# Optimization experiments

Measured on AMD Instinct MI355X. Metric: run time of the kernel, lower is better.

The kernel has to match this reference:

```python
import jax, jax.numpy as jnp
import numpy as np

NT, NP = 100000, 20000
FT, FP, H = 128, 64, 128
E, EL = 2000000, 500000
EPS = 1e-12


def _l2norm(x):
    # F.normalize(x, p=2, dim=-1): x / max(||x||, eps)
    n = jnp.sqrt(jnp.sum(x * x, axis=-1, keepdims=True))
    return x / jnp.maximum(n, EPS)


def _seg_mean(x_src, src_idx, dst_idx, n_dst, inv_cnt):
    # gather src features per edge, scatter-sum to dst, divide by in-degree
    s = jax.ops.segment_sum(x_src[src_idx], dst_idx, num_segments=n_dst)
    return s * inv_cnt[:, None]


def setup_inputs() -> dict:
    key = jax.random.key(0)
    ks = jax.random.split(key, 24)

    def w(k, fan_in, fan_out):
        return jax.random.normal(k, (fan_in, fan_out), jnp.float32) / np.sqrt(fan_in)

    inp = {
        "x_track": jax.random.normal(ks[0], (NT, FT), jnp.float32),
        "x_playlist": jax.random.normal(ks[1], (NP, FP), jnp.float32),
        "edge_src": jax.random.randint(ks[2], (E,), 0, NT),
        "edge_dst": jax.random.randint(ks[3], (E,), 0, NP),
        "label_src": jax.random.randint(ks[4], (EL,), 0, NT),
        "label_dst": jax.random.randint(ks[5], (EL,), 0, NP),
        # per-type input projections (PyG Linear, bias=True)
        "Wn_t": w(ks[6], FT, H), "bn_t": jnp.zeros((H,), jnp.float32),
        "Wn_p": w(ks[7], FP, H), "bn_p": jnp.zeros((H,), jnp.float32),
        # layer1: edge type track->playlist (dst playlist) and reverse (dst track)
        "W1_l_p": w(ks[8], H, H), "b1_p": jnp.zeros((H,), jnp.float32), "W1_r_p": w(ks[9], H, H),
        "W1_l_t": w(ks[10], H, H), "b1_t": jnp.zeros((H,), jnp.float32), "W1_r_t": w(ks[11], H, H),
        # layer2
        "W2_l_p": w(ks[12], H, H), "b2_p": jnp.zeros((H,), jnp.float32), "W2_r_p": w(ks[13], H, H),
        "W2_l_t": w(ks[14], H, H), "b2_t": jnp.zeros((H,), jnp.float32), "W2_r_t": w(ks[15], H, H),
    }
    return inp


def reference(x_track, x_playlist, edge_src, edge_dst, label_src, label_dst,
              Wn_t, bn_t, Wn_p, bn_p,
              W1_l_p, b1_p, W1_r_p, W1_l_t, b1_t, W1_r_t,
              W2_l_p, b2_p, W2_r_p, W2_l_t, b2_t, W2_r_t):
    nt, np_ = x_track.shape[0], x_playlist.shape[0]
    ones = jnp.ones(edge_src.shape, jnp.float32)
    inv_cnt_p = 1.0 / jnp.maximum(jax.ops.segment_sum(ones, edge_dst, num_segments=np_), 1.0)
    inv_cnt_t = 1.0 / jnp.maximum(jax.ops.segment_sum(ones, edge_src, num_segments=nt), 1.0)

    # per-type input linear
    h_t = x_track @ Wn_t + bn_t        # [NT, H]
    h_p = x_playlist @ Wn_p + bn_p     # [NP, H]

    # hetero SAGE layer 1 (normalize=True) + relu
    agg_p = _seg_mean(h_t, edge_src, edge_dst, np_, inv_cnt_p)  # track -> playlist
    agg_t = _seg_mean(h_p, edge_dst, edge_src, nt, inv_cnt_t)   # playlist -> track (rev edges)
    o_p = jax.nn.relu(_l2norm(agg_p @ W1_l_p + b1_p + h_p @ W1_r_p))
    o_t = jax.nn.relu(_l2norm(agg_t @ W1_l_t + b1_t + h_t @ W1_r_t))

    # hetero SAGE layer 2 (normalize=True), no relu
    agg_p2 = _seg_mean(o_t, edge_src, edge_dst, np_, inv_cnt_p)
    agg_t2 = _seg_mean(o_p, edge_dst, edge_src, nt, inv_cnt_t)
    z_p = _l2norm(agg_p2 @ W2_l_p + b2_p + o_p @ W2_r_p)
    z_t = _l2norm(agg_t2 @ W2_l_t + b2_t + o_t @ W2_r_t)

    # link predictor: dot product of endpoint embeddings
    return jnp.sum(z_t[label_src] * z_p[label_dst], axis=-1)  # [EL]
```

## Files before the change

kernel.cpp:

```cpp
#include <hip/hip_runtime.h>
#include <hip/hip_bf16.h>

#define H 128

typedef __attribute__((ext_vector_type(8))) _Float16 f16x8;
typedef __attribute__((ext_vector_type(4))) float f32x4;

static inline size_t align_up(size_t x, size_t a){ return (x + a - 1) & ~(a - 1); }

__device__ inline f32x4 mfma16h(f16x8 a, f16x8 b, f32x4 c){
  return __builtin_amdgcn_mfma_f32_16x16x32_f16(a, b, c, 0, 0, 0);
}

__device__ inline void gload_lds16(const void* g, void* l){
  __builtin_amdgcn_global_load_lds(
      (const __attribute__((address_space(1))) void*)g,
      (__attribute__((address_space(3))) void*)l, 16, 0, 0);
}

struct PackArgs {
  const float* src[10];
  _Float16* dst[10];
  int K[10];
  int start[11];
};

__global__ __launch_bounds__(256) void pack_hist(PackArgs pa, int nblk_pack,
    const int* __restrict__ src, const int* __restrict__ dst, int E,
    int* __restrict__ cnt_b_p, int* __restrict__ cnt_b_t, int histgrid){
  if ((int)blockIdx.x < nblk_pack){
    int t = blockIdx.x * 256 + threadIdx.x;
    if (t >= pa.start[10]) return;
    int m = 0;
    #pragma unroll
    for (int i = 1; i < 10; i++) if (t >= pa.start[i]) m = i;
    int local = t - pa.start[m];
    int k = local >> 7, n = local & 127;
    float w = pa.src[m][local];
    pa.dst[m][n * pa.K[m] + k] = (_Float16)w;
  } else {
    int bid = (int)blockIdx.x - nblk_pack;
    __shared__ int hp[256], ht[256];
    int tid = threadIdx.x;
    hp[tid] = 0; ht[tid] = 0;
    __syncthreads();
    for (int i = bid * 256 + tid; i < E; i += histgrid * 256){
      atomicAdd(&hp[dst[i] >> 7], 1);
      atomicAdd(&ht[src[i] >> 9], 1);
    }
    __syncthreads();
    if (hp[tid]) atomicAdd(&cnt_b_p[tid], hp[tid]);
    if (ht[tid]) atomicAdd(&cnt_b_t[tid], ht[tid]);
  }
}

__global__ void scan_buckets(const int* __restrict__ cb_p, const int* __restrict__ cb_t, int nbp, int nbt,
                             int* __restrict__ base_p, int* __restrict__ base_t,
                             int* __restrict__ cur_p, int* __restrict__ cur_t){
  if (threadIdx.x == 0){
    int s = 0;
    for (int i = 0; i < nbp; i++){ base_p[i] = s; cur_p[i] = s; s += cb_p[i]; }
    base_p[nbp] = s;
  } else if (threadIdx.x == 1){
    int s = 0;
    for (int i = 0; i < nbt; i++){ base_t[i] = s; cur_t[i] = s; s += cb_t[i]; }
    base_t[nbt] = s;
  }
}

__device__ inline void bin_body(const int* __restrict__ keys, const int* __restrict__ vals,
    int E, int shift, int nb, int* __restrict__ cursor, unsigned* __restrict__ rec_out, int chunk,
    int* hist, int* excl, int* gbase, unsigned* recs, unsigned char* binid){
  const int CH = 4096, IT = 16;
  int tid = threadIdx.x;
  int start = chunk * CH;
  int cnt = E - start; if (cnt > CH) cnt = CH;
  if (cnt <= 0) return;
  hist[tid] = 0;
  __syncthreads();
  int b[IT]; int rank[IT]; unsigned rc[IT];
  unsigned mask = (1u << shift) - 1u;
  #pragma unroll
  for (int q = 0; q < IT; q++){
    int i = tid + q * 256;
    if (i < cnt){
      int k = keys[start + i], v = vals[start + i];
      b[q] = k >> shift;
      rc[q] = ((unsigned)v << shift) | ((unsigned)k & mask);
      rank[q] = atomicAdd(&hist[b[q]], 1);
    } else b[q] = -1;
  }
  __syncthreads();
  int lane = tid & 63, wid = tid >> 6;
  if (wid == 0){
    int h0 = hist[lane*4], h1 = hist[lane*4+1], h2 = hist[lane*4+2], h3 = hist[lane*4+3];
    int s = h0 + h1 + h2 + h3;
    int sc = s;
    #pragma unroll
    for (int o = 1; o < 64; o <<= 1){ int t = __shfl_up(sc, (unsigned)o, 64); if (lane >= o) sc += t; }
    int base = sc - s;
    excl[lane*4] = base; excl[lane*4+1] = base + h0;
    excl[lane*4+2] = base + h0 + h1; excl[lane*4+3] = base + h0 + h1 + h2;
  }
  __syncthreads();
  #pragma unroll
  for (int q = 0; q < IT; q++){
    if (b[q] >= 0){
      int pos = excl[b[q]] + rank[q];
      recs[pos] = rc[q];
      binid[pos] = (unsigned char)b[q];
    }
  }
  if (tid < nb && hist[tid] > 0) gbase[tid] = atomicAdd(&cursor[tid], hist[tid]);
  __syncthreads();
  for (int i = tid; i < cnt; i += 256){
    int bb = binid[i];
    rec_out[gbase[bb] + (i - excl[bb])] = recs[i];
  }
}

__global__ __launch_bounds__(256) void bin2(const int* __restrict__ esrc, const int* __restrict__ edst,
    int E, int nb_p, int* cu_p, unsigned* rec_p, int nb_t, int* cu_t, unsigned* rec_t, int nchunks){
  __shared__ int hist[256];
  __shared__ int excl[256];
  __shared__ int gbase[256];
  __shared__ unsigned recs[4096];
  __shared__ unsigned char binid[4096];
  if ((int)blockIdx.x < nchunks)
    bin_body(edst, esrc, E, 7, nb_p, cu_p, rec_p, blockIdx.x, hist, excl, gbase, recs, binid);
  else
    bin_body(esrc, edst, E, 9, nb_t, cu_t, rec_t, blockIdx.x - nchunks, hist, excl, gbase, recs, binid);
}

template<int LOC, int LB>
__device__ inline void build_body(const unsigned* __restrict__ rec, const int* __restrict__ bbase,
    int nkeys, int E, int* __restrict__ off, float* __restrict__ inv, int* __restrict__ csr,
    int b, int nb, int* hist, int* excl, int* cur, int* wsum){
  int tid = threadIdx.x;
  int s = bbase[b], e = bbase[b + 1];
  for (int k = tid; k < LOC; k += 256){ hist[k] = 0; cur[k] = 0; }
  __syncthreads();
  for (int i = s + tid; i < e; i += 256) atomicAdd(&hist[rec[i] & (LOC - 1)], 1);
  __syncthreads();
  int lane = tid & 63, wid = tid >> 6;
  constexpr int BPT = (LOC + 255) / 256;
  int h[BPT]; int ssum = 0;
  #pragma unroll
  for (int q = 0; q < BPT; q++){
    int k = tid * BPT + q;
    h[q] = (k < LOC) ? hist[k] : 0;
    ssum += h[q];
  }
  int sc = ssum;
  #pragma unroll
  for (int o = 1; o < 64; o <<= 1){ int t = __shfl_up(sc, (unsigned)o, 64); if (lane >= o) sc += t; }
  if (lane == 63) wsum[wid] = sc;
  __syncthreads();
  int base = 0;
  for (int w = 0; w < wid; w++) base += wsum[w];
  int ex = base + sc - ssum;
  #pragma unroll
  for (int q = 0; q < BPT; q++){
    int k = tid * BPT + q;
    if (k < LOC) excl[k] = ex;
    ex += h[q];
  }
  __syncthreads();
  int keybase = b << LB;
  for (int k = tid; k < LOC; k += 256){
    int gk = keybase + k;
    if (gk < nkeys){
      off[gk] = s + excl[k];
      int c = hist[k];
      inv[gk] = 1.0f / (float)(c > 1 ? c : 1);
    }
  }
  if (b == nb - 1 && tid == 0) off[nkeys] = E;
  for (int i = s + tid; i < e; i += 256){
    unsigned r = rec[i];
    int k = (int)(r & (LOC - 1));
    int rk = atomicAdd(&cur[k], 1);
    csr[s + excl[k] + rk] = (int)(r >> LB);
  }
}

__global__ __launch_bounds__(256) void build2(
    const unsigned* rec_p, const int* bb_p, int NPk, int* off_p, float* inv_p, int* csr_p, int nb_p,
    const unsigned* rec_t, const int* bb_t, int NTk, int* off_t, float* inv_t, int* csr_t, int nb_t, int E){
  __shared__ int hist[512];
  __shared__ int excl[512];
  __shared__ int cur[512];
  __shared__ int wsum[8];
  if ((int)blockIdx.x < nb_p)
    build_body<128,7>(rec_p, bb_p, NPk, E, off_p, inv_p, csr_p, blockIdx.x, nb_p, hist, excl, cur, wsum);
  else
    build_body<512,9>(rec_t, bb_t, NTk, E, off_t, inv_t, csr_t, blockIdx.x - nb_p, nb_t, hist, excl, cur, wsum);
}

struct ProjJob {
  const float* A;
  const _Float16* WT;
  const float* bias;
  _Float16* OUT;
  int M;
  int ntiles;
  int nblk;
};
template<int KA>
__device__ inline void proj_body(ProjJob j, int bid, char* lds){
  constexpr int KST = KA / 32;
  constexpr int RB_A = KA * 4;
  constexpr int CHA = RB_A / 16;
  constexpr int NIA = 64 * CHA / 512;
  constexpr int ABYTES = 64 * RB_A;

  const int t    = threadIdx.x;
  const int wid  = t >> 6;
  const int lane = t & 63;
  const int l15  = lane & 15;
  const int lkg  = lane >> 4;
  const int colg = wid * 16 + l15;
  const int M = j.M, ntiles = j.ntiles, nblk = j.nblk;

  f16x8 wl[KST];
  {
    const _Float16* bh = j.WT + (size_t)colg * KA + lkg * 8;
    #pragma unroll
    for (int ks = 0; ks < KST; ks++) wl[ks] = *(const f16x8*)(bh + ks * 32);
  }
  const float bb = j.bias[colg];

  auto stage = [&](int tile, char* dstA){
    int row0 = tile * 64;
    #pragma unroll
    for (int q = 0; q < NIA; q++){
      int lc  = q * 512 + t;
      int row = lc / CHA;
      int ch  = lc - row * CHA;
      int grow = row0 + row; if (grow > M - 1) grow = M - 1;
      int gch = ch ^ (row & 7);
      gload_lds16((const char*)j.A + (size_t)grow * RB_A + gch * 16, dstA + lc * 16);
    }
  };

  int p = 0;
  if (bid < ntiles) stage(bid, lds);

  for (int t0 = bid; t0 < ntiles; t0 += nblk){
    const int row0 = t0 * 64;
    const int tn = t0 + nblk;
    const bool hasnext = tn < ntiles;
    if (hasnext) stage(tn, lds + (p ^ 1) * ABYTES);

    if (hasnext){
      if constexpr (NIA == 4) asm volatile("s_waitcnt vmcnt(4)" ::: "memory");
      else                    asm volatile("s_waitcnt vmcnt(2)" ::: "memory");
    } else {
      asm volatile("s_waitcnt vmcnt(0)" ::: "memory");
    }
    __builtin_amdgcn_s_barrier();
    asm volatile("" ::: "memory");

    const char* bufA = lds + p * ABYTES;

    f32x4 acc[4];
    #pragma unroll
    for (int tt = 0; tt < 4; tt++){
      acc[tt] = (f32x4){0.f, 0.f, 0.f, 0.f};
      const int rl = tt * 16 + l15;
      const int sw = rl & 7;
      const char* ap = bufA + rl * RB_A;
      #pragma unroll
      for (int ks = 0; ks < KST; ks++){
        int c0 = lkg * 2 + ks * 8;
        f32x4 a0 = *(const f32x4*)(ap + ((c0    ) ^ sw) * 16);
        f32x4 a1 = *(const f32x4*)(ap + ((c0 + 1) ^ sw) * 16);
        f16x8 af;
        #pragma unroll
        for (int e = 0; e < 8; e++) af[e] = (_Float16)(e < 4 ? a0[e] : a1[e - 4]);
        acc[tt] = mfma16h(af, wl[ks], acc[tt]);
      }
      acc[tt].x += bb; acc[tt].y += bb; acc[tt].z += bb; acc[tt].w += bb;
    }

    #pragma unroll
    for (int tt = 0; tt < 4; tt++){
      #pragma unroll
      for (int r = 0; r < 4; r++){
        int row = row0 + tt * 16 + lkg * 4 + r;
        if (row < M) j.OUT[(size_t)row * H + colg] = (_Float16)acc[tt][r];
      }
    }
    asm volatile("s_waitcnt lgkmcnt(0)" ::: "memory");
    __builtin_amdgcn_s_barrier();
    asm volatile("" ::: "memory");
    p ^= 1;
  }
}
__global__ __launch_bounds__(512) void proj2(ProjJob jt, ProjJob jp){
  __shared__ __align__(16) char lds[2 * 64 * 512];
  if ((int)blockIdx.x < jt.nblk) proj_body<128>(jt, blockIdx.x, lds);
  else                           proj_body<64>(jp, (int)blockIdx.x - jt.nblk, lds);
}

struct SageJob {
  const _Float16* A;
  const _Float16* Bs;
  const _Float16* WlT;
  const _Float16* WrT;
  const float* bias;
  _Float16* OUT;
  int M;
  int ntiles;
  int nblk;
};
template<bool RELU>
__global__ __launch_bounds__(512, 8) void sage_mfma2(SageJob j0, SageJob j1){
  constexpr int KST = 4;
  constexpr int CHA = 16;
  constexpr int NIA = 2, NIB = 2;
  constexpr int ABYTES = 64 * 256;
  constexpr int BUFB = 2 * ABYTES;

  __shared__ __align__(16) char lds[2 * BUFB];
  __shared__ float red[8][64];

  const bool second = (int)blockIdx.x >= j0.nblk;
  const SageJob j = second ? j1 : j0;
  const int bid = (int)blockIdx.x - (second ? j0.nblk : 0);
  const int M = j.M, ntiles = j.ntiles, nblk = j.nblk;

  const int t    = threadIdx.x;
  const int wid  = t >> 6;
  const int lane = t & 63;
  const int l15  = lane & 15;
  const int lkg  = lane >> 4;
  const int colg = wid * 16 + l15;

  f16x8 wl[KST], wr[KST];
  {
    const _Float16* bh  = j.WlT + (size_t)colg * 128 + lkg * 8;
    const _Float16* bh2 = j.WrT + (size_t)colg * 128 + lkg * 8;
    #pragma unroll
    for (int ks = 0; ks < KST; ks++){
      wl[ks] = *(const f16x8*)(bh + ks * 32);
      wr[ks] = *(const f16x8*)(bh2 + ks * 32);
    }
  }
  const float bb = j.bias[colg];

  auto stage = [&](int tile, char* dstA, char* dstB){
    int row0 = tile * 64;
    #pragma unroll
    for (int q = 0; q < NIA; q++){
      int lc  = q * 512 + t;
      int row = lc / CHA;
      int ch  = lc - row * CHA;
      int grow = row0 + row; if (grow > M - 1) grow = M - 1;
      int gch = ch ^ (row & 7);
      gload_lds16((const char*)j.A + (size_t)grow * 256 + gch * 16, dstA + lc * 16);
    }
    #pragma unroll
    for (int q = 0; q < NIB; q++){
      int lc  = q * 512 + t;
      int row = lc >> 4;
      int ch  = lc & 15;
      int grow = row0 + row; if (grow > M - 1) grow = M - 1;
      int gch = ch ^ (row & 7);
      gload_lds16((const char*)j.Bs + (size_t)grow * 256 + gch * 16, dstB + lc * 16);
    }
  };

  int p = 0;
  if (bid < ntiles) stage(bid, lds, lds + ABYTES);

  for (int t0 = bid; t0 < ntiles; t0 += nblk){
    const int row0 = t0 * 64;
    const int tn = t0 + nblk;
    const bool hasnext = tn < ntiles;
    if (hasnext) stage(tn, lds + (p ^ 1) * BUFB, lds + (p ^ 1) * BUFB + ABYTES);

    if (hasnext) asm volatile("s_waitcnt vmcnt(4)" ::: "memory");
    else         asm volatile("s_waitcnt vmcnt(0)" ::: "memory");
    __builtin_amdgcn_s_barrier();
    asm volatile("" ::: "memory");

    const char* bufA = lds + p * BUFB;
    const char* bufB = bufA + ABYTES;

    f32x4 acc[4];
    #pragma unroll
    for (int tt = 0; tt < 4; tt++){
      acc[tt] = (f32x4){0.f, 0.f, 0.f, 0.f};
      const int rl = tt * 16 + l15;
      const int sw = rl & 7;
      const char* ap = bufA + rl * 256;
      #pragma unroll
      for (int ks = 0; ks < KST; ks++){
        f16x8 af = *(const f16x8*)(ap + ((ks * 4 + lkg) ^ sw) * 16);
        acc[tt] = mfma16h(af, wl[ks], acc[tt]);
      }
      const char* bp = bufB + rl * 256;
      #pragma unroll
      for (int ks = 0; ks < KST; ks++){
        f16x8 bf = *(const f16x8*)(bp + ((ks * 4 + lkg) ^ sw) * 16);
        acc[tt] = mfma16h(bf, wr[ks], acc[tt]);
      }
      acc[tt].x += bb; acc[tt].y += bb; acc[tt].z += bb; acc[tt].w += bb;
    }

    #pragma unroll
    for (int tt = 0; tt < 4; tt++){
      #pragma unroll
      for (int r = 0; r < 4; r++){
        float v = acc[tt][r] * acc[tt][r];
        v += __shfl_xor(v, 1, 64);
        v += __shfl_xor(v, 2, 64);
        v += __shfl_xor(v, 4, 64);
        v += __shfl_xor(v, 8, 64);
        if (l15 == 0) red[wid][tt * 16 + lkg * 4 + r] = v;
      }
    }
    asm volatile("s_waitcnt lgkmcnt(0)" ::: "memory");
    __builtin_amdgcn_s_barrier();
    asm volatile("" ::: "memory");
    #pragma unroll
    for (int tt = 0; tt < 4; tt++){
      #pragma unroll
      for (int r = 0; r < 4; r++){
        int idx = tt * 16 + lkg * 4 + r;
        float s = 0.f;
        #pragma unroll
        for (int w2 = 0; w2 < 8; w2++) s += red[w2][idx];
        float scale = 1.f / fmaxf(sqrtf(s), 1e-12f);
        float v = acc[tt][r] * scale;
        if (RELU) v = fmaxf(v, 0.f);
        acc[tt][r] = v;
      }
    }
    #pragma unroll
    for (int tt = 0; tt < 4; tt++){
      #pragma unroll
      for (int r = 0; r < 4; r++){
        int row = row0 + tt * 16 + lkg * 4 + r;
        if (row < M) j.OUT[(size_t)row * H + colg] = (_Float16)acc[tt][r];
      }
    }
    p ^= 1;
  }
}

struct AggJob {
  const _Float16* feat;
  const int* csr;
  const int* off;
  const float* inv;
  _Float16* out;
  int n;
  int nblk;
};
__global__ __launch_bounds__(256) void agg2_kernel(AggJob j0, AggJob j1){
  const bool second = (int)blockIdx.x >= j0.nblk;
  const AggJob j = second ? j1 : j0;
  const int bid = (int)blockIdx.x - (second ? j0.nblk : 0);
  int g = bid * 16 + (threadIdx.x >> 4);
  int l = threadIdx.x & 15;
  if (g >= j.n) return;
  int s = j.off[g], e = j.off[g + 1];
  float c0[8], c1[8], c2[8], c3[8];
  #pragma unroll
  for (int q = 0; q < 8; q++){ c0[q] = 0.f; c1[q] = 0.f; c2[q] = 0.f; c3[q] = 0.f; }
  const _Float16* F = j.feat;
  int i = s;
  for (; i + 3 < e; i += 4){
    f16x8 v0 = *(const f16x8*)(F + (size_t)j.csr[i]     * H + l * 8);
    f16x8 v1 = *(const f16x8*)(F + (size_t)j.csr[i + 1] * H + l * 8);
    f16x8 v2 = *(const f16x8*)(F + (size_t)j.csr[i + 2] * H + l * 8);
    f16x8 v3 = *(const f16x8*)(F + (size_t)j.csr[i + 3] * H + l * 8);
    #pragma unroll
    for (int q = 0; q < 8; q++){
      c0[q] += (float)v0[q]; c1[q] += (float)v1[q];
      c2[q] += (float)v2[q]; c3[q] += (float)v3[q];
    }
  }
  for (; i < e; i++){
    f16x8 v0 = *(const f16x8*)(F + (size_t)j.csr[i] * H + l * 8);
    #pragma unroll
    for (int q = 0; q < 8; q++) c0[q] += (float)v0[q];
  }
  float iv = j.inv[g];
  f16x8 ov;
  #pragma unroll
  for (int q = 0; q < 8; q++){
    float r = (c0[q] + c1[q]) + (c2[q] + c3[q]);
    ov[q] = (_Float16)(r * iv);
  }
  *(f16x8*)(j.out + (size_t)g * H + l * 8) = ov;
}

__global__ __launch_bounds__(256) void dot_kernel(const _Float16* __restrict__ zt, const _Float16* __restrict__ zp,
                           const int* __restrict__ ls, const int* __restrict__ ld,
                           float* __restrict__ out, int n){
  int w = (blockIdx.x * 256 + threadIdx.x) >> 4;
  int l = threadIdx.x & 15;
  if (w >= n) return;
  f16x8 x = *(const f16x8*)&zt[(size_t)ls[w] * H + l * 8];
  f16x8 y = *(const f16x8*)&zp[(size_t)ld[w] * H + l * 8];
  float v = 0.f;
  #pragma unroll
  for (int q = 0; q < 8; q++) v += (float)x[q] * (float)y[q];
  v += __shfl_xor(v, 1, 64);
  v += __shfl_xor(v, 2, 64);
  v += __shfl_xor(v, 4, 64);
  v += __shfl_xor(v, 8, 64);
  if (l == 0) out[w] = v;
}

extern "C" void kernel_launch(void* const* d_in, const int* in_sizes, int n_in,
                              void* d_out, int out_size, void* d_ws, size_t ws_size,
                              hipStream_t stream){
  const float* x_t  = (const float*)d_in[0];
  const float* x_p  = (const float*)d_in[1];
  const int*   esrc = (const int*)d_in[2];
  const int*   edst = (const int*)d_in[3];
  const int*   lsrc = (const int*)d_in[4];
  const int*   ldst = (const int*)d_in[5];
  const float* Wn_t = (const float*)d_in[6];
  const float* bn_t = (const float*)d_in[7];
  const float* Wn_p = (const float*)d_in[8];
  const float* bn_p = (const float*)d_in[9];
  const float* W1_l_p=(const float*)d_in[10]; const float* b1_p=(const float*)d_in[11]; const float* W1_r_p=(const float*)d_in[12];
  const float* W1_l_t=(const float*)d_in[13]; const float* b1_t=(const float*)d_in[14]; const float* W1_r_t=(const float*)d_in[15];
  const float* W2_l_p=(const float*)d_in[16]; const float* b2_p=(const float*)d_in[17]; const float* W2_r_p=(const float*)d_in[18];
  const float* W2_l_t=(const float*)d_in[19]; const float* b2_t=(const float*)d_in[20]; const float* W2_r_t=(const float*)d_in[21];
  float* out = (float*)d_out;

  const int FT = 128, FP = 64;
  int NT = in_sizes[0] / FT;
  int NP = in_sizes[1] / FP;
  int E  = in_sizes[2];
  int EL = in_sizes[4];

  const int SH_P = 7, SH_T = 9;
  int nb_p = (NP + (1 << SH_P) - 1) >> SH_P;
  int nb_t = (NT + (1 << SH_T) - 1) >> SH_T;

  char* base = (char*)d_ws;
  size_t o = 0;
  auto alloc = [&](size_t bytes) -> char* { char* p = base + o; o = align_up(o + bytes, 256); return p; };
  int*   cb_p  = (int*)alloc(256 * 4);
  int*   cb_t  = (int*)alloc(256 * 4);
  size_t zero_bytes = o;
  int*   bb_p  = (int*)alloc(260 * 4);
  int*   bb_t  = (int*)alloc(260 * 4);
  int*   cu_p  = (int*)alloc(256 * 4);
  int*   cu_t  = (int*)alloc(256 * 4);
  int*   off_p = (int*)alloc((size_t)(NP + 1) * 4);
  int*   off_t = (int*)alloc((size_t)(NT + 1) * 4);
  float* inv_p = (float*)alloc((size_t)NP * 4);
  float* inv_t = (float*)alloc((size_t)NT * 4);
  unsigned* rec_p = (unsigned*)alloc((size_t)E * 4);
  unsigned* rec_t = (unsigned*)alloc((size_t)E * 4);
  int*   csr_p = (int*)alloc((size_t)E * 4);
  int*   csr_t = (int*)alloc((size_t)E * 4);
  _Float16* h_t = (_Float16*)alloc((size_t)NT * H * 2);
  _Float16* h_p = (_Float16*)alloc((size_t)NP * H * 2);
  _Float16* a_t = (_Float16*)alloc((size_t)NT * H * 2);
  _Float16* a_p = (_Float16*)alloc((size_t)NP * H * 2);

  PackArgs pa;
  const float* wsrc[10] = {Wn_t, Wn_p, W1_l_p, W1_r_p, W1_l_t, W1_r_t, W2_l_p, W2_r_p, W2_l_t, W2_r_t};
  int Ks[10] = {128, 64, 128, 128, 128, 128, 128, 128, 128, 128};
  _Float16* wpk[10];
  int st = 0;
  for (int m = 0; m < 10; m++){
    wpk[m] = (_Float16*)alloc((size_t)128 * Ks[m] * 2);
    pa.src[m] = wsrc[m]; pa.dst[m] = wpk[m]; pa.K[m] = Ks[m]; pa.start[m] = st;
    st += Ks[m] * 128;
  }
  pa.start[10] = st;
  (void)ws_size; (void)n_in; (void)out_size;

  hipMemsetAsync(base, 0, zero_bytes, stream);

  int nblk_pack = (st + 255) / 256;
  const int histgrid = 512;
  pack_hist<<<nblk_pack + histgrid, 256, 0, stream>>>(pa, nblk_pack, esrc, edst, E, cb_p, cb_t, histgrid);
  scan_buckets<<<1, 64, 0, stream>>>(cb_p, cb_t, nb_p, nb_t, bb_p, bb_t, cu_p, cu_t);
  int nchunks = (E + 4095) / 4096;
  bin2<<<2 * nchunks, 256, 0, stream>>>(esrc, edst, E, nb_p, cu_p, rec_p, nb_t, cu_t, rec_t, nchunks);
  build2<<<nb_p + nb_t, 256, 0, stream>>>(rec_p, bb_p, NP, off_p, inv_p, csr_p, nb_p,
                                          rec_t, bb_t, NT, off_t, inv_t, csr_t, nb_t, E);

  int tiles_t = (NT + 63) / 64;
  int tiles_p = (NP + 63) / 64;
  int pblk_t = tiles_t < 448 ? tiles_t : 448;
  int pblk_p = tiles_p < 64 ? tiles_p : 64;
  ProjJob pjt{x_t, wpk[0], bn_t, h_t, NT, tiles_t, pblk_t};
  ProjJob pjp{x_p, wpk[1], bn_p, h_p, NP, tiles_p, pblk_p};
  proj2<<<pblk_t + pblk_p, 512, 0, stream>>>(pjt, pjp);

  int ablk_p = (NP + 15) / 16;
  int ablk_t = (NT + 15) / 16;
  AggJob aj_p1{h_t, csr_p, off_p, inv_p, a_p, NP, ablk_p};
  AggJob aj_t1{h_p, csr_t, off_t, inv_t, a_t, NT, ablk_t};
  AggJob aj_p2{a_t, csr_p, off_p, inv_p, h_p, NP, ablk_p};
  AggJob aj_t2{a_p, csr_t, off_t, inv_t, h_t, NT, ablk_t};

  int nblk_p = tiles_p < 96 ? tiles_p : 96;
  int nblk_t = tiles_t < 416 ? tiles_t : 416;
  SageJob sj1p{a_p, h_p, wpk[2], wpk[3], b1_p, a_p, NP, tiles_p, nblk_p};
  SageJob sj1t{a_t, h_t, wpk[4], wpk[5], b1_t, a_t, NT, tiles_t, nblk_t};
  SageJob sj2p{h_p, a_p, wpk[6], wpk[7], b2_p, h_p, NP, tiles_p, nblk_p};
  SageJob sj2t{h_t, a_t, wpk[8], wpk[9], b2_t, h_t, NT, tiles_t, nblk_t};

  agg2_kernel<<<ablk_p + ablk_t, 256, 0, stream>>>(aj_p1, aj_t1);
  sage_mfma2<true><<<nblk_p + nblk_t, 512, 0, stream>>>(sj1p, sj1t);

  agg2_kernel<<<ablk_p + ablk_t, 256, 0, stream>>>(aj_p2, aj_t2);
  sage_mfma2<false><<<nblk_p + nblk_t, 512, 0, stream>>>(sj2p, sj2t);

  dot_kernel<<<(EL + 15) / 16, 256, 0, stream>>>(h_t, h_p, lsrc, ldst, out, EL);
}
```

Measured before the change: 494.2 us.

## Bucket label edges by track index so the dot kernel reads z_t with locality

Adds a histogram, scan and binning pass for the label edges, keyed on label_src in 512-row buckets, reusing the existing edge-binning machinery. The dot kernel then walks each bucket in chunks, so gathers of track embeddings hit a small, cache-resident window instead of random rows. The cost is extra work in the histogram and bin kernels and an indirect index load per label. Packing the label index into the record leaves 23 bits (index shifted left by 9), which fits EL=500000.

```diff
diff --git a/kernel.cpp b/kernel.cpp
--- a/kernel.cpp
+++ b/kernel.cpp
@@ -27,7 +27,8 @@
 
 __global__ __launch_bounds__(256) void pack_hist(PackArgs pa, int nblk_pack,
     const int* __restrict__ src, const int* __restrict__ dst, int E,
-    int* __restrict__ cnt_b_p, int* __restrict__ cnt_b_t, int histgrid){
+    const int* __restrict__ lsrc, int EL,
+    int* __restrict__ cnt_b_p, int* __restrict__ cnt_b_t, int* __restrict__ cnt_b_l, int histgrid){
   if ((int)blockIdx.x < nblk_pack){
     int t = blockIdx.x * 256 + threadIdx.x;
     if (t >= pa.start[10]) return;
@@ -40,23 +41,28 @@
     pa.dst[m][n * pa.K[m] + k] = (_Float16)w;
   } else {
     int bid = (int)blockIdx.x - nblk_pack;
-    __shared__ int hp[256], ht[256];
+    __shared__ int hp[256], ht[256], hl[256];
     int tid = threadIdx.x;
-    hp[tid] = 0; ht[tid] = 0;
+    hp[tid] = 0; ht[tid] = 0; hl[tid] = 0;
     __syncthreads();
     for (int i = bid * 256 + tid; i < E; i += histgrid * 256){
       atomicAdd(&hp[dst[i] >> 7], 1);
       atomicAdd(&ht[src[i] >> 9], 1);
     }
+    for (int i = bid * 256 + tid; i < EL; i += histgrid * 256){
+      atomicAdd(&hl[lsrc[i] >> 9], 1);
+    }
     __syncthreads();
     if (hp[tid]) atomicAdd(&cnt_b_p[tid], hp[tid]);
     if (ht[tid]) atomicAdd(&cnt_b_t[tid], ht[tid]);
-  }
-}
-
-__global__ void scan_buckets(const int* __restrict__ cb_p, const int* __restrict__ cb_t, int nbp, int nbt,
-                             int* __restrict__ base_p, int* __restrict__ base_t,
-                             int* __restrict__ cur_p, int* __restrict__ cur_t){
+    if (hl[tid]) atomicAdd(&cnt_b_l[tid], hl[tid]);
+  }
+}
+
+__global__ void scan_buckets(const int* __restrict__ cb_p, const int* __restrict__ cb_t,
+                             const int* __restrict__ cb_l, int nbp, int nbt, int nbl,
+                             int* __restrict__ base_p, int* __restrict__ base_t, int* __restrict__ base_l,
+                             int* __restrict__ cur_p, int* __restrict__ cur_t, int* __restrict__ cur_l){
   if (threadIdx.x == 0){
     int s = 0;
     for (int i = 0; i < nbp; i++){ base_p[i] = s; cur_p[i] = s; s += cb_p[i]; }
@@ -65,6 +71,10 @@
     int s = 0;
     for (int i = 0; i < nbt; i++){ base_t[i] = s; cur_t[i] = s; s += cb_t[i]; }
     base_t[nbt] = s;
+  } else if (threadIdx.x == 2){
+    int s = 0;
+    for (int i = 0; i < nbl; i++){ base_l[i] = s; cur_l[i] = s; s += cb_l[i]; }
+    base_l[nbl] = s;
   }
 }
 
@@ -84,7 +94,8 @@
   for (int q = 0; q < IT; q++){
     int i = tid + q * 256;
     if (i < cnt){
-      int k = keys[start + i], v = vals[start + i];
+      int k = keys[start + i];
+      int v = vals ? vals[start + i] : (start + i);
       b[q] = k >> shift;
       rc[q] = ((unsigned)v << shift) | ((unsigned)k & mask);
       rank[q] = atomicAdd(&hist[b[q]], 1);
@@ -119,8 +130,9 @@
   }
 }
 
-__global__ __launch_bounds__(256) void bin2(const int* __restrict__ esrc, const int* __restrict__ edst,
-    int E, int nb_p, int* cu_p, unsigned* rec_p, int nb_t, int* cu_t, unsigned* rec_t, int nchunks){
+__global__ __launch_bounds__(256) void bin3(const int* __restrict__ esrc, const int* __restrict__ edst,
+    int E, int nb_p, int* cu_p, unsigned* rec_p, int nb_t, int* cu_t, unsigned* rec_t, int nchunks,
+    const int* __restrict__ lsrc, int EL, int nb_l, int* cu_l, unsigned* rec_l, int nchunks_l){
   __shared__ int hist[256];
   __shared__ int excl[256];
   __shared__ int gbase[256];
@@ -128,8 +140,10 @@
   __shared__ unsigned char binid[4096];
   if ((int)blockIdx.x < nchunks)
     bin_body(edst, esrc, E, 7, nb_p, cu_p, rec_p, blockIdx.x, hist, excl, gbase, recs, binid);
+  else if ((int)blockIdx.x < 2 * nchunks)
+    bin_body(esrc, edst, E, 9, nb_t, cu_t, rec_t, blockIdx.x - nchunks, hist, excl, gbase, recs, binid);
   else
-    bin_body(esrc, edst, E, 9, nb_t, cu_t, rec_t, blockIdx.x - nchunks, hist, excl, gbase, recs, binid);
+    bin_body(lsrc, nullptr, EL, 9, nb_l, cu_l, rec_l, blockIdx.x - 2 * nchunks, hist, excl, gbase, recs, binid);
 }
 
 template<int LOC, int LB>
@@ -499,21 +513,32 @@
 }
 
 __global__ __launch_bounds__(256) void dot_kernel(const _Float16* __restrict__ zt, const _Float16* __restrict__ zp,
-                           const int* __restrict__ ls, const int* __restrict__ ld,
-                           float* __restrict__ out, int n){
-  int w = (blockIdx.x * 256 + threadIdx.x) >> 4;
+                           const unsigned* __restrict__ rec_l, const int* __restrict__ base_l,
+                           const int* __restrict__ ld, float* __restrict__ out, int CPB){
+  int b = blockIdx.x / CPB;
+  int c = blockIdx.x - b * CPB;
+  int s = base_l[b], e = base_l[b + 1];
+  int len = e - s;
+  int cs = s + (int)(((long long)len * c) / CPB);
+  int ce = s + (int)(((long long)len * (c + 1)) / CPB);
+  int g = threadIdx.x >> 4;
   int l = threadIdx.x & 15;
-  if (w >= n) return;
-  f16x8 x = *(const f16x8*)&zt[(size_t)ls[w] * H + l * 8];
-  f16x8 y = *(const f16x8*)&zp[(size_t)ld[w] * H + l * 8];
-  float v = 0.f;
-  #pragma unroll
-  for (int q = 0; q < 8; q++) v += (float)x[q] * (float)y[q];
-  v += __shfl_xor(v, 1, 64);
-  v += __shfl_xor(v, 2, 64);
-  v += __shfl_xor(v, 4, 64);
-  v += __shfl_xor(v, 8, 64);
-  if (l == 0) out[w] = v;
+  for (int i = cs + g; i < ce; i += 16){
+    unsigned r = rec_l[i];
+    int idx = (int)(r >> 9);
+    int src = (b << 9) | (int)(r & 511u);
+    int dst = ld[idx];
+    f16x8 x = *(const f16x8*)&zt[(size_t)src * H + l * 8];
+    f16x8 y = *(const f16x8*)&zp[(size_t)dst * H + l * 8];
+    float v = 0.f;
+    #pragma unroll
+    for (int q = 0; q < 8; q++) v += (float)x[q] * (float)y[q];
+    v += __shfl_xor(v, 1, 64);
+    v += __shfl_xor(v, 2, 64);
+    v += __shfl_xor(v, 4, 64);
+    v += __shfl_xor(v, 8, 64);
+    if (l == 0) out[idx] = v;
+  }
 }
 
 extern "C" void kernel_launch(void* const* d_in, const int* in_sizes, int n_in,
@@ -544,23 +569,28 @@
   const int SH_P = 7, SH_T = 9;
   int nb_p = (NP + (1 << SH_P) - 1) >> SH_P;
   int nb_t = (NT + (1 << SH_T) - 1) >> SH_T;
+  int nb_l = (NT + 511) >> 9;
 
   char* base = (char*)d_ws;
   size_t o = 0;
   auto alloc = [&](size_t bytes) -> char* { char* p = base + o; o = align_up(o + bytes, 256); return p; };
   int*   cb_p  = (int*)alloc(256 * 4);
   int*   cb_t  = (int*)alloc(256 * 4);
+  int*   cb_l  = (int*)alloc(256 * 4);
   size_t zero_bytes = o;
   int*   bb_p  = (int*)alloc(260 * 4);
   int*   bb_t  = (int*)alloc(260 * 4);
+  int*   bb_l  = (int*)alloc(260 * 4);
   int*   cu_p  = (int*)alloc(256 * 4);
   int*   cu_t  = (int*)alloc(256 * 4);
+  int*   cu_l  = (int*)alloc(256 * 4);
   int*   off_p = (int*)alloc((size_t)(NP + 1) * 4);
   int*   off_t = (int*)alloc((size_t)(NT + 1) * 4);
   float* inv_p = (float*)alloc((size_t)NP * 4);
   float* inv_t = (float*)alloc((size_t)NT * 4);
   unsigned* rec_p = (unsigned*)alloc((size_t)E * 4);
   unsigned* rec_t = (unsigned*)alloc((size_t)E * 4);
+  unsigned* rec_l = (unsigned*)alloc((size_t)EL * 4);
   int*   csr_p = (int*)alloc((size_t)E * 4);
   int*   csr_t = (int*)alloc((size_t)E * 4);
   _Float16* h_t = (_Float16*)alloc((size_t)NT * H * 2);
@@ -585,10 +615,14 @@
 
   int nblk_pack = (st + 255) / 256;
   const int histgrid = 512;
-  pack_hist<<<nblk_pack + histgrid, 256, 0, stream>>>(pa, nblk_pack, esrc, edst, E, cb_p, cb_t, histgrid);
-  scan_buckets<<<1, 64, 0, stream>>>(cb_p, cb_t, nb_p, nb_t, bb_p, bb_t, cu_p, cu_t);
+  pack_hist<<<nblk_pack + histgrid, 256, 0, stream>>>(pa, nblk_pack, esrc, edst, E, lsrc, EL,
+                                                      cb_p, cb_t, cb_l, histgrid);
+  scan_buckets<<<1, 64, 0, stream>>>(cb_p, cb_t, cb_l, nb_p, nb_t, nb_l,
+                                     bb_p, bb_t, bb_l, cu_p, cu_t, cu_l);
   int nchunks = (E + 4095) / 4096;
-  bin2<<<2 * nchunks, 256, 0, stream>>>(esrc, edst, E, nb_p, cu_p, rec_p, nb_t, cu_t, rec_t, nchunks);
+  int nchunks_l = (EL + 4095) / 4096;
+  bin3<<<2 * nchunks + nchunks_l, 256, 0, stream>>>(esrc, edst, E, nb_p, cu_p, rec_p, nb_t, cu_t, rec_t, nchunks,
+                                                    lsrc, EL, nb_l, cu_l, rec_l, nchunks_l);
   build2<<<nb_p + nb_t, 256, 0, stream>>>(rec_p, bb_p, NP, off_p, inv_p, csr_p, nb_p,
                                           rec_t, bb_t, NT, off_t, inv_t, csr_t, nb_t, E);
 
@@ -620,5 +654,6 @@
   agg2_kernel<<<ablk_p + ablk_t, 256, 0, stream>>>(aj_p2, aj_t2);
   sage_mfma2<false><<<nblk_p + nblk_t, 512, 0, stream>>>(sj2p, sj2t);
 
-  dot_kernel<<<(EL + 15) / 16, 256, 0, stream>>>(h_t, h_p, lsrc, ldst, out, EL);
-}
+  const int CPB = 10;
+  dot_kernel<<<nb_l * CPB, 256, 0, stream>>>(h_t, h_p, rec_l, bb_l, ldst, out, CPB);
+}
```

Measured after the change: 517.6 us. 4.7% more time.

## Fuse weight pack, edge histogram and input projection into one kernel

Applied to the files above, without the earlier changes.

Merges the weight-packing/histogram kernel and the input projection kernel into a single launch, with blocks dispatched by index range. The projection now reads the fp32 weights directly and converts them in registers, so it no longer depends on the packed copies. This lets the projection run concurrently with the histogram work and removes one kernel launch and a dependency. The cost is a strided, uncoalesced weight load per block, plus a larger launch with 512-thread blocks for the pack and histogram paths.

```diff
diff --git a/kernel.cpp b/kernel.cpp
--- a/kernel.cpp
+++ b/kernel.cpp
@@ -25,181 +25,9 @@
   int start[11];
 };
 
-__global__ __launch_bounds__(256) void pack_hist(PackArgs pa, int nblk_pack,
-    const int* __restrict__ src, const int* __restrict__ dst, int E,
-    int* __restrict__ cnt_b_p, int* __restrict__ cnt_b_t, int histgrid){
-  if ((int)blockIdx.x < nblk_pack){
-    int t = blockIdx.x * 256 + threadIdx.x;
-    if (t >= pa.start[10]) return;
-    int m = 0;
-    #pragma unroll
-    for (int i = 1; i < 10; i++) if (t >= pa.start[i]) m = i;
-    int local = t - pa.start[m];
-    int k = local >> 7, n = local & 127;
-    float w = pa.src[m][local];
-    pa.dst[m][n * pa.K[m] + k] = (_Float16)w;
-  } else {
-    int bid = (int)blockIdx.x - nblk_pack;
-    __shared__ int hp[256], ht[256];
-    int tid = threadIdx.x;
-    hp[tid] = 0; ht[tid] = 0;
-    __syncthreads();
-    for (int i = bid * 256 + tid; i < E; i += histgrid * 256){
-      atomicAdd(&hp[dst[i] >> 7], 1);
-      atomicAdd(&ht[src[i] >> 9], 1);
-    }
-    __syncthreads();
-    if (hp[tid]) atomicAdd(&cnt_b_p[tid], hp[tid]);
-    if (ht[tid]) atomicAdd(&cnt_b_t[tid], ht[tid]);
-  }
-}
-
-__global__ void scan_buckets(const int* __restrict__ cb_p, const int* __restrict__ cb_t, int nbp, int nbt,
-                             int* __restrict__ base_p, int* __restrict__ base_t,
-                             int* __restrict__ cur_p, int* __restrict__ cur_t){
-  if (threadIdx.x == 0){
-    int s = 0;
-    for (int i = 0; i < nbp; i++){ base_p[i] = s; cur_p[i] = s; s += cb_p[i]; }
-    base_p[nbp] = s;
-  } else if (threadIdx.x == 1){
-    int s = 0;
-    for (int i = 0; i < nbt; i++){ base_t[i] = s; cur_t[i] = s; s += cb_t[i]; }
-    base_t[nbt] = s;
-  }
-}
-
-__device__ inline void bin_body(const int* __restrict__ keys, const int* __restrict__ vals,
-    int E, int shift, int nb, int* __restrict__ cursor, unsigned* __restrict__ rec_out, int chunk,
-    int* hist, int* excl, int* gbase, unsigned* recs, unsigned char* binid){
-  const int CH = 4096, IT = 16;
-  int tid = threadIdx.x;
-  int start = chunk * CH;
-  int cnt = E - start; if (cnt > CH) cnt = CH;
-  if (cnt <= 0) return;
-  hist[tid] = 0;
-  __syncthreads();
-  int b[IT]; int rank[IT]; unsigned rc[IT];
-  unsigned mask = (1u << shift) - 1u;
-  #pragma unroll
-  for (int q = 0; q < IT; q++){
-    int i = tid + q * 256;
-    if (i < cnt){
-      int k = keys[start + i], v = vals[start + i];
-      b[q] = k >> shift;
-      rc[q] = ((unsigned)v << shift) | ((unsigned)k & mask);
-      rank[q] = atomicAdd(&hist[b[q]], 1);
-    } else b[q] = -1;
-  }
-  __syncthreads();
-  int lane = tid & 63, wid = tid >> 6;
-  if (wid == 0){
-    int h0 = hist[lane*4], h1 = hist[lane*4+1], h2 = hist[lane*4+2], h3 = hist[lane*4+3];
-    int s = h0 + h1 + h2 + h3;
-    int sc = s;
-    #pragma unroll
-    for (int o = 1; o < 64; o <<= 1){ int t = __shfl_up(sc, (unsigned)o, 64); if (lane >= o) sc += t; }
-    int base = sc - s;
-    excl[lane*4] = base; excl[lane*4+1] = base + h0;
-    excl[lane*4+2] = base + h0 + h1; excl[lane*4+3] = base + h0 + h1 + h2;
-  }
-  __syncthreads();
-  #pragma unroll
-  for (int q = 0; q < IT; q++){
-    if (b[q] >= 0){
-      int pos = excl[b[q]] + rank[q];
-      recs[pos] = rc[q];
-      binid[pos] = (unsigned char)b[q];
-    }
-  }
-  if (tid < nb && hist[tid] > 0) gbase[tid] = atomicAdd(&cursor[tid], hist[tid]);
-  __syncthreads();
-  for (int i = tid; i < cnt; i += 256){
-    int bb = binid[i];
-    rec_out[gbase[bb] + (i - excl[bb])] = recs[i];
-  }
-}
-
-__global__ __launch_bounds__(256) void bin2(const int* __restrict__ esrc, const int* __restrict__ edst,
-    int E, int nb_p, int* cu_p, unsigned* rec_p, int nb_t, int* cu_t, unsigned* rec_t, int nchunks){
-  __shared__ int hist[256];
-  __shared__ int excl[256];
-  __shared__ int gbase[256];
-  __shared__ unsigned recs[4096];
-  __shared__ unsigned char binid[4096];
-  if ((int)blockIdx.x < nchunks)
-    bin_body(edst, esrc, E, 7, nb_p, cu_p, rec_p, blockIdx.x, hist, excl, gbase, recs, binid);
-  else
-    bin_body(esrc, edst, E, 9, nb_t, cu_t, rec_t, blockIdx.x - nchunks, hist, excl, gbase, recs, binid);
-}
-
-template<int LOC, int LB>
-__device__ inline void build_body(const unsigned* __restrict__ rec, const int* __restrict__ bbase,
-    int nkeys, int E, int* __restrict__ off, float* __restrict__ inv, int* __restrict__ csr,
-    int b, int nb, int* hist, int* excl, int* cur, int* wsum){
-  int tid = threadIdx.x;
-  int s = bbase[b], e = bbase[b + 1];
-  for (int k = tid; k < LOC; k += 256){ hist[k] = 0; cur[k] = 0; }
-  __syncthreads();
-  for (int i = s + tid; i < e; i += 256) atomicAdd(&hist[rec[i] & (LOC - 1)], 1);
-  __syncthreads();
-  int lane = tid & 63, wid = tid >> 6;
-  constexpr int BPT = (LOC + 255) / 256;
-  int h[BPT]; int ssum = 0;
-  #pragma unroll
-  for (int q = 0; q < BPT; q++){
-    int k = tid * BPT + q;
-    h[q] = (k < LOC) ? hist[k] : 0;
-    ssum += h[q];
-  }
-  int sc = ssum;
-  #pragma unroll
-  for (int o = 1; o < 64; o <<= 1){ int t = __shfl_up(sc, (unsigned)o, 64); if (lane >= o) sc += t; }
-  if (lane == 63) wsum[wid] = sc;
-  __syncthreads();
-  int base = 0;
-  for (int w = 0; w < wid; w++) base += wsum[w];
-  int ex = base + sc - ssum;
-  #pragma unroll
-  for (int q = 0; q < BPT; q++){
-    int k = tid * BPT + q;
-    if (k < LOC) excl[k] = ex;
-    ex += h[q];
-  }
-  __syncthreads();
-  int keybase = b << LB;
-  for (int k = tid; k < LOC; k += 256){
-    int gk = keybase + k;
-    if (gk < nkeys){
-      off[gk] = s + excl[k];
-      int c = hist[k];
-      inv[gk] = 1.0f / (float)(c > 1 ? c : 1);
-    }
-  }
-  if (b == nb - 1 && tid == 0) off[nkeys] = E;
-  for (int i = s + tid; i < e; i += 256){
-    unsigned r = rec[i];
-    int k = (int)(r & (LOC - 1));
-    int rk = atomicAdd(&cur[k], 1);
-    csr[s + excl[k] + rk] = (int)(r >> LB);
-  }
-}
-
-__global__ __launch_bounds__(256) void build2(
-    const unsigned* rec_p, const int* bb_p, int NPk, int* off_p, float* inv_p, int* csr_p, int nb_p,
-    const unsigned* rec_t, const int* bb_t, int NTk, int* off_t, float* inv_t, int* csr_t, int nb_t, int E){
-  __shared__ int hist[512];
-  __shared__ int excl[512];
-  __shared__ int cur[512];
-  __shared__ int wsum[8];
-  if ((int)blockIdx.x < nb_p)
-    build_body<128,7>(rec_p, bb_p, NPk, E, off_p, inv_p, csr_p, blockIdx.x, nb_p, hist, excl, cur, wsum);
-  else
-    build_body<512,9>(rec_t, bb_t, NTk, E, off_t, inv_t, csr_t, blockIdx.x - nb_p, nb_t, hist, excl, cur, wsum);
-}
-
 struct ProjJob {
   const float* A;
-  const _Float16* WT;
+  const float* Wsrc;
   const float* bias;
   _Float16* OUT;
   int M;
@@ -223,10 +51,11 @@
   const int M = j.M, ntiles = j.ntiles, nblk = j.nblk;
 
   f16x8 wl[KST];
-  {
-    const _Float16* bh = j.WT + (size_t)colg * KA + lkg * 8;
-    #pragma unroll
-    for (int ks = 0; ks < KST; ks++) wl[ks] = *(const f16x8*)(bh + ks * 32);
+  #pragma unroll
+  for (int ks = 0; ks < KST; ks++){
+    #pragma unroll
+    for (int e = 0; e < 8; e++)
+      wl[ks][e] = (_Float16)j.Wsrc[(size_t)(lkg * 8 + ks * 32 + e) * 128 + colg];
   }
   const float bb = j.bias[colg];
 
@@ -297,10 +126,188 @@
     p ^= 1;
   }
 }
-__global__ __launch_bounds__(512) void proj2(ProjJob jt, ProjJob jp){
+
+__global__ __launch_bounds__(512) void mega1(PackArgs pa, int nblk_pack,
+    const int* __restrict__ esrc, const int* __restrict__ edst, int E,
+    int* __restrict__ cnt_b_p, int* __restrict__ cnt_b_t, int histgrid,
+    ProjJob jt, ProjJob jp){
   __shared__ __align__(16) char lds[2 * 64 * 512];
-  if ((int)blockIdx.x < jt.nblk) proj_body<128>(jt, blockIdx.x, lds);
-  else                           proj_body<64>(jp, (int)blockIdx.x - jt.nblk, lds);
+  int bid = (int)blockIdx.x;
+  if (bid < nblk_pack){
+    int t = bid * 512 + threadIdx.x;
+    if (t >= pa.start[10]) return;
+    int m = 0;
+    #pragma unroll
+    for (int i = 1; i < 10; i++) if (t >= pa.start[i]) m = i;
+    int local = t - pa.start[m];
+    int k = local >> 7, n = local & 127;
+    pa.dst[m][n * pa.K[m] + k] = (_Float16)pa.src[m][local];
+    return;
+  }
+  bid -= nblk_pack;
+  if (bid < histgrid){
+    int* hp = (int*)lds;
+    int* ht = hp + 256;
+    int tid = threadIdx.x;
+    if (tid < 256){ hp[tid] = 0; ht[tid] = 0; }
+    __syncthreads();
+    for (int i = bid * 512 + tid; i < E; i += histgrid * 512){
+      atomicAdd(&hp[edst[i] >> 7], 1);
+      atomicAdd(&ht[esrc[i] >> 9], 1);
+    }
+    __syncthreads();
+    if (tid < 256){
+      if (hp[tid]) atomicAdd(&cnt_b_p[tid], hp[tid]);
+      if (ht[tid]) atomicAdd(&cnt_b_t[tid], ht[tid]);
+    }
+    return;
+  }
+  bid -= histgrid;
+  if (bid < jt.nblk) proj_body<128>(jt, bid, lds);
+  else               proj_body<64>(jp, bid - jt.nblk, lds);
+}
+
+__global__ void scan_buckets(const int* __restrict__ cb_p, const int* __restrict__ cb_t, int nbp, int nbt,
+                             int* __restrict__ base_p, int* __restrict__ base_t,
+                             int* __restrict__ cur_p, int* __restrict__ cur_t){
+  if (threadIdx.x == 0){
+    int s = 0;
+    for (int i = 0; i < nbp; i++){ base_p[i] = s; cur_p[i] = s; s += cb_p[i]; }
+    base_p[nbp] = s;
+  } else if (threadIdx.x == 1){
+    int s = 0;
+    for (int i = 0; i < nbt; i++){ base_t[i] = s; cur_t[i] = s; s += cb_t[i]; }
+    base_t[nbt] = s;
+  }
+}
+
+__device__ inline void bin_body(const int* __restrict__ keys, const int* __restrict__ vals,
+    int E, int shift, int nb, int* __restrict__ cursor, unsigned* __restrict__ rec_out, int chunk,
+    int* hist, int* excl, int* gbase, unsigned* recs, unsigned char* binid){
+  const int CH = 4096, IT = 16;
+  int tid = threadIdx.x;
+  int start = chunk * CH;
+  int cnt = E - start; if (cnt > CH) cnt = CH;
+  if (cnt <= 0) return;
+  hist[tid] = 0;
+  __syncthreads();
+  int b[IT]; int rank[IT]; unsigned rc[IT];
+  unsigned mask = (1u << shift) - 1u;
+  #pragma unroll
+  for (int q = 0; q < IT; q++){
+    int i = tid + q * 256;
+    if (i < cnt){
+      int k = keys[start + i], v = vals[start + i];
+      b[q] = k >> shift;
+      rc[q] = ((unsigned)v << shift) | ((unsigned)k & mask);
+      rank[q] = atomicAdd(&hist[b[q]], 1);
+    } else b[q] = -1;
+  }
+  __syncthreads();
+  int lane = tid & 63, wid = tid >> 6;
+  if (wid == 0){
+    int h0 = hist[lane*4], h1 = hist[lane*4+1], h2 = hist[lane*4+2], h3 = hist[lane*4+3];
+    int s = h0 + h1 + h2 + h3;
+    int sc = s;
+    #pragma unroll
+    for (int o = 1; o < 64; o <<= 1){ int t = __shfl_up(sc, (unsigned)o, 64); if (lane >= o) sc += t; }
+    int base = sc - s;
+    excl[lane*4] = base; excl[lane*4+1] = base + h0;
+    excl[lane*4+2] = base + h0 + h1; excl[lane*4+3] = base + h0 + h1 + h2;
+  }
+  __syncthreads();
+  #pragma unroll
+  for (int q = 0; q < IT; q++){
+    if (b[q] >= 0){
+      int pos = excl[b[q]] + rank[q];
+      recs[pos] = rc[q];
+      binid[pos] = (unsigned char)b[q];
+    }
+  }
+  if (tid < nb && hist[tid] > 0) gbase[tid] = atomicAdd(&cursor[tid], hist[tid]);
+  __syncthreads();
+  for (int i = tid; i < cnt; i += 256){
+    int bb = binid[i];
+    rec_out[gbase[bb] + (i - excl[bb])] = recs[i];
+  }
+}
+
+__global__ __launch_bounds__(256) void bin2(const int* __restrict__ esrc, const int* __restrict__ edst,
+    int E, int nb_p, int* cu_p, unsigned* rec_p, int nb_t, int* cu_t, unsigned* rec_t, int nchunks){
+  __shared__ int hist[256];
+  __shared__ int excl[256];
+  __shared__ int gbase[256];
+  __shared__ unsigned recs[4096];
+  __shared__ unsigned char binid[4096];
+  if ((int)blockIdx.x < nchunks)
+    bin_body(edst, esrc, E, 7, nb_p, cu_p, rec_p, blockIdx.x, hist, excl, gbase, recs, binid);
+  else
+    bin_body(esrc, edst, E, 9, nb_t, cu_t, rec_t, blockIdx.x - nchunks, hist, excl, gbase, recs, binid);
+}
+
+template<int LOC, int LB>
+__device__ inline void build_body(const unsigned* __restrict__ rec, const int* __restrict__ bbase,
+    int nkeys, int E, int* __restrict__ off, float* __restrict__ inv, int* __restrict__ csr,
+    int b, int nb, int* hist, int* excl, int* cur, int* wsum){
+  int tid = threadIdx.x;
+  int s = bbase[b], e = bbase[b + 1];
+  for (int k = tid; k < LOC; k += 256){ hist[k] = 0; cur[k] = 0; }
+  __syncthreads();
+  for (int i = s + tid; i < e; i += 256) atomicAdd(&hist[rec[i] & (LOC - 1)], 1);
+  __syncthreads();
+  int lane = tid & 63, wid = tid >> 6;
+  constexpr int BPT = (LOC + 255) / 256;
+  int h[BPT]; int ssum = 0;
+  #pragma unroll
+  for (int q = 0; q < BPT; q++){
+    int k = tid * BPT + q;
+    h[q] = (k < LOC) ? hist[k] : 0;
+    ssum += h[q];
+  }
+  int sc = ssum;
+  #pragma unroll
+  for (int o = 1; o < 64; o <<= 1){ int t = __shfl_up(sc, (unsigned)o, 64); if (lane >= o) sc += t; }
+  if (lane == 63) wsum[wid] = sc;
+  __syncthreads();
+  int base = 0;
+  for (int w = 0; w < wid; w++) base += wsum[w];
+  int ex = base + sc - ssum;
+  #pragma unroll
+  for (int q = 0; q < BPT; q++){
+    int k = tid * BPT + q;
+    if (k < LOC) excl[k] = ex;
+    ex += h[q];
+  }
+  __syncthreads();
+  int keybase = b << LB;
+  for (int k = tid; k < LOC; k += 256){
+    int gk = keybase + k;
+    if (gk < nkeys){
+      off[gk] = s + excl[k];
+      int c = hist[k];
+      inv[gk] = 1.0f / (float)(c > 1 ? c : 1);
+    }
+  }
+  if (b == nb - 1 && tid == 0) off[nkeys] = E;
+  for (int i = s + tid; i < e; i += 256){
+    unsigned r = rec[i];
+    int k = (int)(r & (LOC - 1));
+    int rk = atomicAdd(&cur[k], 1);
+    csr[s + excl[k] + rk] = (int)(r >> LB);
+  }
+}
+
+__global__ __launch_bounds__(256) void build2(
+    const unsigned* rec_p, const int* bb_p, int NPk, int* off_p, float* inv_p, int* csr_p, int nb_p,
+    const unsigned* rec_t, const int* bb_t, int NTk, int* off_t, float* inv_t, int* csr_t, int nb_t, int E){
+  __shared__ int hist[512];
+  __shared__ int excl[512];
+  __shared__ int cur[512];
+  __shared__ int wsum[8];
+  if ((int)blockIdx.x < nb_p)
+    build_body<128,7>(rec_p, bb_p, NPk, E, off_p, inv_p, csr_p, blockIdx.x, nb_p, hist, excl, cur, wsum);
+  else
+    build_body<512,9>(rec_t, bb_t, NTk, E, off_t, inv_t, csr_t, blockIdx.x - nb_p, nb_t, hist, excl, cur, wsum);
 }
 
 struct SageJob {
@@ -583,22 +590,22 @@
 
   hipMemsetAsync(base, 0, zero_bytes, stream);
 
-  int nblk_pack = (st + 255) / 256;
+  int tiles_t = (NT + 63) / 64;
+  int tiles_p = (NP + 63) / 64;
+  int pblk_t = tiles_t < 448 ? tiles_t : 448;
+  int pblk_p = tiles_p < 64 ? tiles_p : 64;
+  ProjJob pjt{x_t, Wn_t, bn_t, h_t, NT, tiles_t, pblk_t};
+  ProjJob pjp{x_p, Wn_p, bn_p, h_p, NP, tiles_p, pblk_p};
+  int nblk_pack = (st + 511) / 512;
   const int histgrid = 512;
-  pack_hist<<<nblk_pack + histgrid, 256, 0, stream>>>(pa, nblk_pack, esrc, edst, E, cb_p, cb_t, histgrid);
+  mega1<<<nblk_pack + histgrid + pblk_t + pblk_p, 512, 0, stream>>>(
+      pa, nblk_pack, esrc, edst, E, cb_p, cb_t, histgrid, pjt, pjp);
+
   scan_buckets<<<1, 64, 0, stream>>>(cb_p, cb_t, nb_p, nb_t, bb_p, bb_t, cu_p, cu_t);
   int nchunks = (E + 4095) / 4096;
   bin2<<<2 * nchunks, 256, 0, stream>>>(esrc, edst, E, nb_p, cu_p, rec_p, nb_t, cu_t, rec_t, nchunks);
   build2<<<nb_p + nb_t, 256, 0, stream>>>(rec_p, bb_p, NP, off_p, inv_p, csr_p, nb_p,
                                           rec_t, bb_t, NT, off_t, inv_t, csr_t, nb_t, E);
-
-  int tiles_t = (NT + 63) / 64;
-  int tiles_p = (NP + 63) / 64;
-  int pblk_t = tiles_t < 448 ? tiles_t : 448;
-  int pblk_p = tiles_p < 64 ? tiles_p : 64;
-  ProjJob pjt{x_t, wpk[0], bn_t, h_t, NT, tiles_t, pblk_t};
-  ProjJob pjp{x_p, wpk[1], bn_p, h_p, NP, tiles_p, pblk_p};
-  proj2<<<pblk_t + pblk_p, 512, 0, stream>>>(pjt, pjp);
 
   int ablk_p = (NP + 15) / 16;
   int ablk_t = (NT + 15) / 16;
```

After: 488.4 us. No clear change (-1.2%).
